# Optimization experiments

Measured on AMD Instinct MI355X. Metric: run time of the kernel, lower is better.

## Reference

```python
import jax, jax.numpy as jnp
import numpy as np

EPS = 1e-5
N, K, C = 32768, 27, 128


def setup_inputs() -> dict:
    key = jax.random.key(0)
    k1, k2, k3, k4 = jax.random.split(key, 4)
    feats = jax.random.normal(k1, (N, C), dtype=jnp.float32)
    # Precomputed kernel-offset neighbor map (MinkowskiEngine kernel map),
    # one input index per (point, kernel offset).
    neighbors = jax.random.randint(k2, (N, K), 0, N, dtype=jnp.int32)
    scale = 1.0 / np.sqrt(K * C)  # fan-in init like sparse conv
    W1 = jax.random.normal(k3, (K, C, C), dtype=jnp.float32) * scale
    W2 = jax.random.normal(k4, (K, C, C), dtype=jnp.float32) * scale
    g1 = jnp.ones((C,), jnp.float32)
    b1 = jnp.zeros((C,), jnp.float32)
    g2 = jnp.ones((C,), jnp.float32)
    b2 = jnp.zeros((C,), jnp.float32)
    return {"feats": feats, "neighbors": neighbors, "W1": W1, "g1": g1,
            "b1": b1, "W2": W2, "g2": g2, "b2": b2}


def _sparse_conv(f, nbr, W):
    # gather-GEMM-scatter: gather neighbor features per kernel offset,
    # contract with that offset's weight, sum over offsets.
    gathered = f[nbr]                      # [N, K, C]
    return jnp.einsum('nkc,kcd->nd', gathered, W)  # [N, C]


def _batch_norm(x, gamma, beta):
    mu = jnp.mean(x, axis=0)
    var = jnp.mean(jnp.square(x - mu), axis=0)
    return (x - mu) * jax.lax.rsqrt(var + EPS) * gamma + beta


def reference(feats, neighbors, W1, g1, b1, W2, g2, b2):
    out = _sparse_conv(feats, neighbors, W1)
    out = jax.nn.relu(_batch_norm(out, g1, b1))
    out = _sparse_conv(out, neighbors, W2)
    out = _batch_norm(out, g2, b2)
    return jax.nn.relu(out + feats)
```

## Files before the change

kernel.cpp:

```cpp
#include <hip/hip_runtime.h>
#include <stdint.h>

#define NPTS 32768
#define KOFF 27
#define CH   128
#define NC   (NPTS*CH)
#define KSPLIT 3
#define KPG  9
#define TILE_M 64
#define NITER (KPG*2)

typedef __attribute__((ext_vector_type(8))) short short8;
typedef __attribute__((ext_vector_type(4))) float f32x4;
typedef unsigned short u16;

__device__ __forceinline__ float bf2f(u16 u) {
    union { uint32_t i; float f; } v; v.i = ((uint32_t)u) << 16; return v.f;
}
__device__ __forceinline__ u16 f2bf(float f) {
    union { float f; uint32_t i; } v; v.f = f;
    return (u16)((v.i + 0x7FFF + ((v.i >> 16) & 1)) >> 16);
}

#define GLDS16(gp, lp) __builtin_amdgcn_global_load_lds( \
    (__attribute__((address_space(1))) void*)(gp),           \
    (__attribute__((address_space(3))) void*)(lp), 16, 0, 0)

__global__ __launch_bounds__(256)
void prep_kernel(const float* __restrict__ W1, const float* __restrict__ W2,
                 u16* __restrict__ W1t, u16* __restrict__ W2t,
                 const float* __restrict__ feats, u16* __restrict__ xbuf,
                 float* __restrict__ stat)
{
    __shared__ u16 t[128*129];
    const int b = blockIdx.x, tid = threadIdx.x;
    if (b < 2*KOFF) {
        if (b == 0) for (int i = tid; i < 512; i += 256) stat[i] = 0.0f;
        const float* src = (b < KOFF) ? W1 + (size_t)b*CH*CH : W2 + (size_t)(b-KOFF)*CH*CH;
        u16* dst         = (b < KOFF) ? W1t + (size_t)b*CH*CH : W2t + (size_t)(b-KOFF)*CH*CH;
        for (int e = tid; e < CH*CH; e += 256) {
            int c = e >> 7, d = e & 127;
            t[d*129 + c] = f2bf(src[e]);
        }
        __syncthreads();
        for (int e = tid; e < CH*CH; e += 256) {
            int d = e >> 7, c = e & 127;
            dst[e] = t[d*129 + c];
        }
    } else {
        size_t e = ((size_t)(b - 2*KOFF) * 256 + tid) * 8;
        float4 a = *(const float4*)(feats + e);
        float4 c = *(const float4*)(feats + e + 4);
        ushort4 lo, hi;
        lo.x = f2bf(a.x); lo.y = f2bf(a.y); lo.z = f2bf(a.z); lo.w = f2bf(a.w);
        hi.x = f2bf(c.x); hi.y = f2bf(c.y); hi.z = f2bf(c.z); hi.w = f2bf(c.w);
        *(ushort4*)(xbuf + e) = lo;
        *(ushort4*)(xbuf + e + 4) = hi;
    }
}

__global__ __launch_bounds__(256, 5)
void ResidualBlock_77498389889548_kernel(const u16* __restrict__ xb,
                                         const int* __restrict__ nbr,
                                         const u16* __restrict__ Wt,
                                         u16* __restrict__ part)
{
    __shared__ __align__(16) u16 A_lds[TILE_M*64];
    __shared__ __align__(16) u16 B_lds[CH*64];
    __shared__ int idx_lds[KPG*TILE_M];

    const int tid = threadIdx.x;
    const int n0  = blockIdx.x * TILE_M;
    const int kg  = blockIdx.y;

    for (int e = tid; e < KPG*TILE_M; e += 256) {
        int kk = e >> 6, r = e & 63;
        int nb = nbr[(size_t)(n0 + r)*KOFF + kg*KPG + kk];
        idx_lds[e] = ((unsigned)nb < (unsigned)NPTS) ? nb : 0;
    }
    __syncthreads();

    const int wave = tid >> 6;
    const int lane = tid & 63;
    const int wrow = (wave >> 1) * 32;
    const int wcol = (wave & 1) * 64;
    const int lm   = lane & 15;
    const int quad = lane >> 4;
    const int l8r  = lane >> 3;
    const int swz  = ((lane & 7) ^ l8r) << 3;

    f32x4 acc[2][4];
    #pragma unroll
    for (int i = 0; i < 2; ++i)
        #pragma unroll
        for (int j = 0; j < 4; ++j)
            #pragma unroll
            for (int r = 0; r < 4; ++r) acc[i][j][r] = 0.0f;

    int aoff[2][2], boff[2][4];
    #pragma unroll
    for (int kc = 0; kc < 2; ++kc) {
        int g = kc*4 + quad;
        #pragma unroll
        for (int i = 0; i < 2; ++i) {
            int row = wrow + i*16 + lm;
            aoff[kc][i] = row*128 + ((g ^ (row & 7)) << 4);
        }
        #pragma unroll
        for (int j = 0; j < 4; ++j) {
            int d = wcol + j*16 + lm;
            boff[kc][j] = d*128 + ((g ^ (d & 7)) << 4);
        }
    }

    const char* Ab = (const char*)A_lds;
    const char* Bb = (const char*)B_lds;

    for (int it = 0; it < NITER; ++it) {
        const int kk = it >> 1;
        const int h  = it & 1;

        #pragma unroll
        for (int j = 0; j < 2; ++j) {
            int row8 = wave*16 + j*8;
            int nb = idx_lds[kk*64 + row8 + l8r];
            GLDS16(xb + (size_t)nb*CH + h*64 + swz, &A_lds[row8*64]);
        }
        const u16* wb = Wt + (size_t)(kg*KPG + kk)*CH*CH + h*64 + swz;
        #pragma unroll
        for (int j = 0; j < 4; ++j) {
            int row8 = wave*32 + j*8;
            GLDS16(wb + (size_t)(row8 + l8r)*CH, &B_lds[row8*64]);
        }
        __syncthreads();

        #pragma unroll
        for (int kc = 0; kc < 2; ++kc) {
            short8 a[2], b[4];
            #pragma unroll
            for (int i = 0; i < 2; ++i) a[i] = *(const short8*)(Ab + aoff[kc][i]);
            #pragma unroll
            for (int j = 0; j < 4; ++j) b[j] = *(const short8*)(Bb + boff[kc][j]);
            #pragma unroll
            for (int i = 0; i < 2; ++i)
                #pragma unroll
                for (int j = 0; j < 4; ++j)
                    acc[i][j] = __builtin_amdgcn_mfma_f32_16x16x32_bf16(a[i], b[j], acc[i][j], 0, 0, 0);
        }
        __syncthreads();
    }

    u16* pb = part + (size_t)kg * NC;
    const int colb = wcol + lm;
    #pragma unroll
    for (int i = 0; i < 2; ++i) {
        #pragma unroll
        for (int r = 0; r < 4; ++r) {
            int row = n0 + wrow + i*16 + quad*4 + r;
            u16* pp = pb + (size_t)row*CH + colb;
            #pragma unroll
            for (int j = 0; j < 4; ++j) pp[j*16] = f2bf(acc[i][j][r]);
        }
    }
}

__global__ __launch_bounds__(256)
void sumstats_kernel(const u16* __restrict__ p0, const u16* __restrict__ p1,
                     const u16* __restrict__ p2, u16* __restrict__ y,
                     float* __restrict__ gsum, float* __restrict__ gsq)
{
    __shared__ float ls[CH], lq[CH];
    const int tid = threadIdx.x;
    const int c8 = (tid & 15) * 8;
    const int r0 = tid >> 4;
    const int b = blockIdx.x;
    if (tid < CH) { ls[tid] = 0.0f; lq[tid] = 0.0f; }
    __syncthreads();

    float s[8], q[8];
    #pragma unroll
    for (int i = 0; i < 8; ++i) { s[i] = 0.0f; q[i] = 0.0f; }

    for (int r = r0; r < 128; r += 16) {
        size_t e = (size_t)(b*128 + r)*CH + c8;
        ushort4 a0 = *(const ushort4*)(p0 + e), a1 = *(const ushort4*)(p0 + e + 4);
        ushort4 b0 = *(const ushort4*)(p1 + e), b1 = *(const ushort4*)(p1 + e + 4);
        ushort4 d0 = *(const ushort4*)(p2 + e), d1 = *(const ushort4*)(p2 + e + 4);
        float v[8];
        v[0] = bf2f(a0.x) + bf2f(b0.x) + bf2f(d0.x);
        v[1] = bf2f(a0.y) + bf2f(b0.y) + bf2f(d0.y);
        v[2] = bf2f(a0.z) + bf2f(b0.z) + bf2f(d0.z);
        v[3] = bf2f(a0.w) + bf2f(b0.w) + bf2f(d0.w);
        v[4] = bf2f(a1.x) + bf2f(b1.x) + bf2f(d1.x);
        v[5] = bf2f(a1.y) + bf2f(b1.y) + bf2f(d1.y);
        v[6] = bf2f(a1.z) + bf2f(b1.z) + bf2f(d1.z);
        v[7] = bf2f(a1.w) + bf2f(b1.w) + bf2f(d1.w);
        ushort4 o0, o1;
        o0.x = f2bf(v[0]); o0.y = f2bf(v[1]); o0.z = f2bf(v[2]); o0.w = f2bf(v[3]);
        o1.x = f2bf(v[4]); o1.y = f2bf(v[5]); o1.z = f2bf(v[6]); o1.w = f2bf(v[7]);
        *(ushort4*)(y + e) = o0;
        *(ushort4*)(y + e + 4) = o1;
        #pragma unroll
        for (int i = 0; i < 8; ++i) { s[i] += v[i]; q[i] += v[i]*v[i]; }
    }
    #pragma unroll
    for (int i = 0; i < 8; ++i) {
        atomicAdd(&ls[c8 + i], s[i]);
        atomicAdd(&lq[c8 + i], q[i]);
    }
    __syncthreads();
    if (tid < CH) {
        atomicAdd(&gsum[tid], ls[tid]);
        atomicAdd(&gsq[tid],  lq[tid]);
    }
}

__global__ __launch_bounds__(256)
void norm_relu_kernel(const u16* __restrict__ y, const float* __restrict__ sums,
                      const float* __restrict__ sumsq, const float* __restrict__ gam,
                      const float* __restrict__ bet, u16* __restrict__ xo)
{
    __shared__ float sc[128], sh[128];
    const int tid = threadIdx.x;
    if (tid < 128) {
        float mu  = sums[tid] * (1.0f/NPTS);
        float var = fmaxf(sumsq[tid] * (1.0f/NPTS) - mu*mu, 0.0f);
        float rs  = rsqrtf(var + 1e-5f);
        float s   = rs * gam[tid];
        sc[tid] = s; sh[tid] = bet[tid] - mu*s;
    }
    __syncthreads();
    size_t e = ((size_t)blockIdx.x*256 + tid) * 8;
    int c0 = (int)(e & 127);
    ushort4 lo = *(const ushort4*)(y + e);
    ushort4 hi = *(const ushort4*)(y + e + 4);
    ushort4 o0, o1;
    o0.x = f2bf(fmaxf(bf2f(lo.x)*sc[c0+0] + sh[c0+0], 0.0f));
    o0.y = f2bf(fmaxf(bf2f(lo.y)*sc[c0+1] + sh[c0+1], 0.0f));
    o0.z = f2bf(fmaxf(bf2f(lo.z)*sc[c0+2] + sh[c0+2], 0.0f));
    o0.w = f2bf(fmaxf(bf2f(lo.w)*sc[c0+3] + sh[c0+3], 0.0f));
    o1.x = f2bf(fmaxf(bf2f(hi.x)*sc[c0+4] + sh[c0+4], 0.0f));
    o1.y = f2bf(fmaxf(bf2f(hi.y)*sc[c0+5] + sh[c0+5], 0.0f));
    o1.z = f2bf(fmaxf(bf2f(hi.z)*sc[c0+6] + sh[c0+6], 0.0f));
    o1.w = f2bf(fmaxf(bf2f(hi.w)*sc[c0+7] + sh[c0+7], 0.0f));
    *(ushort4*)(xo + e) = o0;
    *(ushort4*)(xo + e + 4) = o1;
}

__global__ __launch_bounds__(256)
void final_kernel(const u16* __restrict__ y, const float* __restrict__ sums,
                  const float* __restrict__ sumsq, const float* __restrict__ gam,
                  const float* __restrict__ bet, const float* __restrict__ feats,
                  float* __restrict__ out)
{
    __shared__ float sc[128], sh[128];
    const int tid = threadIdx.x;
    if (tid < 128) {
        float mu  = sums[tid] * (1.0f/NPTS);
        float var = fmaxf(sumsq[tid] * (1.0f/NPTS) - mu*mu, 0.0f);
        float rs  = rsqrtf(var + 1e-5f);
        float s   = rs * gam[tid];
        sc[tid] = s; sh[tid] = bet[tid] - mu*s;
    }
    __syncthreads();
    size_t e = ((size_t)blockIdx.x*256 + tid) * 4;
    int c0 = (int)(e & 127);
    ushort4 in = *(const ushort4*)(y + e);
    float4 ft = *(const float4*)(feats + e);
    float4 o;
    o.x = fmaxf(bf2f(in.x)*sc[c0+0] + sh[c0+0] + ft.x, 0.0f);
    o.y = fmaxf(bf2f(in.y)*sc[c0+1] + sh[c0+1] + ft.y, 0.0f);
    o.z = fmaxf(bf2f(in.z)*sc[c0+2] + sh[c0+2] + ft.z, 0.0f);
    o.w = fmaxf(bf2f(in.w)*sc[c0+3] + sh[c0+3] + ft.w, 0.0f);
    *(float4*)(out + e) = o;
}

extern "C" void kernel_launch(void* const* d_in, const int* in_sizes, int n_in,
                              void* d_out, int out_size, void* d_ws, size_t ws_size,
                              hipStream_t stream)
{
    const float* feats = (const float*)d_in[0];
    const int*   nbr   = (const int*)d_in[1];
    const float* W1    = (const float*)d_in[2];
    const float* g1    = (const float*)d_in[3];
    const float* b1    = (const float*)d_in[4];
    const float* W2    = (const float*)d_in[5];
    const float* g2    = (const float*)d_in[6];
    const float* b2    = (const float*)d_in[7];
    float* out = (float*)d_out;

    char* ws = (char*)d_ws;
    u16*   xbuf = (u16*)ws;
    u16*   prt  = xbuf + (size_t)NC;
    u16*   ybuf = prt + (size_t)3*NC;
    u16*   W1t  = ybuf + (size_t)NC;
    u16*   W2t  = W1t + (size_t)KOFF*CH*CH;
    float* stat = (float*)(W2t + (size_t)KOFF*CH*CH);

    prep_kernel<<<dim3(2*KOFF + NC/2048), 256, 0, stream>>>(W1, W2, W1t, W2t, feats, xbuf, stat);

    ResidualBlock_77498389889548_kernel<<<dim3(NPTS/TILE_M, KSPLIT), 256, 0, stream>>>(
        xbuf, nbr, W1t, prt);
    sumstats_kernel<<<dim3(NPTS/128), 256, 0, stream>>>(
        prt, prt + (size_t)NC, prt + (size_t)2*NC, ybuf, stat, stat + 128);
    norm_relu_kernel<<<dim3(NC/2048), 256, 0, stream>>>(ybuf, stat, stat + 128, g1, b1, xbuf);

    ResidualBlock_77498389889548_kernel<<<dim3(NPTS/TILE_M, KSPLIT), 256, 0, stream>>>(
        xbuf, nbr, W2t, prt);
    sumstats_kernel<<<dim3(NPTS/128), 256, 0, stream>>>(
        prt, prt + (size_t)NC, prt + (size_t)2*NC, ybuf, stat + 256, stat + 384);
    final_kernel<<<dim3(NC/1024), 256, 0, stream>>>(ybuf, stat + 256, stat + 384, g2, b2, feats, out);
}
```

Baseline: 222.5 us.

## Fuse partial-sum, BN statistics and normalize via grid barrier; shrink index LDS

Merges the sumstats and normalize/final kernels into one persistent 256-block kernel. Each block keeps its summed tile in LDS, joins a global atomic-counter barrier once the batch statistics are complete, then normalizes straight from LDS. This drops the ybuf round trip through global memory and one launch per BN. It also stores neighbor indices as u16 and raises the GEMM's waves-per-EU hint from 5 to 6 for occupancy. The grid barrier relies on all 256 blocks being co-resident, and the counters are zeroed in the prep kernel each call.

```diff
diff --git a/kernel.cpp b/kernel.cpp
--- a/kernel.cpp
+++ b/kernel.cpp
@@ -9,6 +9,7 @@
 #define KPG  9
 #define TILE_M 64
 #define NITER (KPG*2)
+#define RBLK  256
 
 typedef __attribute__((ext_vector_type(8))) short short8;
 typedef __attribute__((ext_vector_type(4))) float f32x4;
@@ -35,7 +36,7 @@
     __shared__ u16 t[128*129];
     const int b = blockIdx.x, tid = threadIdx.x;
     if (b < 2*KOFF) {
-        if (b == 0) for (int i = tid; i < 512; i += 256) stat[i] = 0.0f;
+        if (b == 0) for (int i = tid; i < 640; i += 256) stat[i] = 0.0f;
         const float* src = (b < KOFF) ? W1 + (size_t)b*CH*CH : W2 + (size_t)(b-KOFF)*CH*CH;
         u16* dst         = (b < KOFF) ? W1t + (size_t)b*CH*CH : W2t + (size_t)(b-KOFF)*CH*CH;
         for (int e = tid; e < CH*CH; e += 256) {
@@ -59,7 +60,7 @@
     }
 }
 
-__global__ __launch_bounds__(256, 5)
+__global__ __launch_bounds__(256, 6)
 void ResidualBlock_77498389889548_kernel(const u16* __restrict__ xb,
                                          const int* __restrict__ nbr,
                                          const u16* __restrict__ Wt,
@@ -67,7 +68,7 @@
 {
     __shared__ __align__(16) u16 A_lds[TILE_M*64];
     __shared__ __align__(16) u16 B_lds[CH*64];
-    __shared__ int idx_lds[KPG*TILE_M];
+    __shared__ u16 idx_lds[KPG*TILE_M];
 
     const int tid = threadIdx.x;
     const int n0  = blockIdx.x * TILE_M;
@@ -76,7 +77,7 @@
     for (int e = tid; e < KPG*TILE_M; e += 256) {
         int kk = e >> 6, r = e & 63;
         int nb = nbr[(size_t)(n0 + r)*KOFF + kg*KPG + kk];
-        idx_lds[e] = ((unsigned)nb < (unsigned)NPTS) ? nb : 0;
+        idx_lds[e] = (u16)(((unsigned)nb < (unsigned)NPTS) ? nb : 0);
     }
     __syncthreads();
 
@@ -123,7 +124,7 @@
         #pragma unroll
         for (int j = 0; j < 2; ++j) {
             int row8 = wave*16 + j*8;
-            int nb = idx_lds[kk*64 + row8 + l8r];
+            int nb = (int)idx_lds[kk*64 + row8 + l8r];
             GLDS16(xb + (size_t)nb*CH + h*64 + swz, &A_lds[row8*64]);
         }
         const u16* wb = Wt + (size_t)(kg*KPG + kk)*CH*CH + h*64 + swz;
@@ -164,115 +165,112 @@
     }
 }
 
+#define FUSED_PROLOGUE(p0, p1, p2, gsum, gsq, ctr)                              \
+    __shared__ u16 vbuf[128*CH];                                     \
+    __shared__ float ls[CH], lq[CH];                                            \
+    const int tid = threadIdx.x;                                                \
+    const int b = blockIdx.x;                                                   \
+    const int c8 = (tid & 15) * 8;                                              \
+    const int r0 = tid >> 4;                                                    \
+    if (tid < CH) { ls[tid] = 0.0f; lq[tid] = 0.0f; }                           \
+    __syncthreads();                                                            \
+    {                                                                           \
+        float s[8], q[8];                                                       \
+        _Pragma("unroll") for (int i = 0; i < 8; ++i) { s[i]=0.0f; q[i]=0.0f; } \
+        for (int i = 0; i < 8; ++i) {                                           \
+            int r = r0 + i*16;                                                  \
+            size_t e = (size_t)(b*128 + r)*CH + c8;                             \
+            ushort4 a0 = *(const ushort4*)(p0 + e), a1 = *(const ushort4*)(p0 + e + 4); \
+            ushort4 b0 = *(const ushort4*)(p1 + e), b1 = *(const ushort4*)(p1 + e + 4); \
+            ushort4 d0 = *(const ushort4*)(p2 + e), d1 = *(const ushort4*)(p2 + e + 4); \
+            float v[8];                                                         \
+            v[0]=bf2f(a0.x)+bf2f(b0.x)+bf2f(d0.x); v[1]=bf2f(a0.y)+bf2f(b0.y)+bf2f(d0.y); \
+            v[2]=bf2f(a0.z)+bf2f(b0.z)+bf2f(d0.z); v[3]=bf2f(a0.w)+bf2f(b0.w)+bf2f(d0.w); \
+            v[4]=bf2f(a1.x)+bf2f(b1.x)+bf2f(d1.x); v[5]=bf2f(a1.y)+bf2f(b1.y)+bf2f(d1.y); \
+            v[6]=bf2f(a1.z)+bf2f(b1.z)+bf2f(d1.z); v[7]=bf2f(a1.w)+bf2f(b1.w)+bf2f(d1.w); \
+            u16* vp = &vbuf[r*CH + c8];                                         \
+            _Pragma("unroll") for (int j = 0; j < 8; ++j) vp[j] = f2bf(v[j]);   \
+            _Pragma("unroll") for (int j = 0; j < 8; ++j) { s[j]+=v[j]; q[j]+=v[j]*v[j]; } \
+        }                                                                       \
+        _Pragma("unroll") for (int j = 0; j < 8; ++j) {                         \
+            atomicAdd(&ls[c8 + j], s[j]); atomicAdd(&lq[c8 + j], q[j]);         \
+        }                                                                       \
+    }                                                                           \
+    __syncthreads();                                                            \
+    if (tid < CH) { atomicAdd(&gsum[tid], ls[tid]); atomicAdd(&gsq[tid], lq[tid]); } \
+    __syncthreads();                                                            \
+    if (tid == 0) {                                                             \
+        __threadfence();                                                        \
+        __hip_atomic_fetch_add(ctr, 1u, __ATOMIC_RELEASE, __HIP_MEMORY_SCOPE_AGENT); \
+        while (__hip_atomic_load(ctr, __ATOMIC_ACQUIRE, __HIP_MEMORY_SCOPE_AGENT) < (unsigned)RBLK) \
+            __builtin_amdgcn_s_sleep(8);                                        \
+    }                                                                           \
+    __syncthreads();                                                            \
+    if (tid < CH) {                                                             \
+        float su = __hip_atomic_load(&gsum[tid], __ATOMIC_RELAXED, __HIP_MEMORY_SCOPE_AGENT); \
+        float sq = __hip_atomic_load(&gsq[tid],  __ATOMIC_RELAXED, __HIP_MEMORY_SCOPE_AGENT); \
+        float mu  = su * (1.0f/NPTS);                                           \
+        float var = fmaxf(sq * (1.0f/NPTS) - mu*mu, 0.0f);                      \
+        float rs  = rsqrtf(var + 1e-5f);                                        \
+        float sf  = rs * gam[tid];                                              \
+        ls[tid] = sf; lq[tid] = bet[tid] - mu*sf;                   \
+    }                                                                           \
+    __syncthreads();
+
 __global__ __launch_bounds__(256)
-void sumstats_kernel(const u16* __restrict__ p0, const u16* __restrict__ p1,
-                     const u16* __restrict__ p2, u16* __restrict__ y,
-                     float* __restrict__ gsum, float* __restrict__ gsq)
-{
-    __shared__ float ls[CH], lq[CH];
-    const int tid = threadIdx.x;
-    const int c8 = (tid & 15) * 8;
-    const int r0 = tid >> 4;
-    const int b = blockIdx.x;
-    if (tid < CH) { ls[tid] = 0.0f; lq[tid] = 0.0f; }
-    __syncthreads();
-
-    float s[8], q[8];
-    #pragma unroll
-    for (int i = 0; i < 8; ++i) { s[i] = 0.0f; q[i] = 0.0f; }
-
-    for (int r = r0; r < 128; r += 16) {
+void fused_norm_kernel(const u16* __restrict__ p0, const u16* __restrict__ p1,
+                       const u16* __restrict__ p2,
+                       float* __restrict__ gsum, float* __restrict__ gsq,
+                       unsigned* __restrict__ ctr,
+                       const float* __restrict__ gam, const float* __restrict__ bet,
+                       u16* __restrict__ xo)
+{
+    FUSED_PROLOGUE(p0, p1, p2, gsum, gsq, ctr)
+    for (int i = 0; i < 8; ++i) {
+        int r = r0 + i*16;
         size_t e = (size_t)(b*128 + r)*CH + c8;
-        ushort4 a0 = *(const ushort4*)(p0 + e), a1 = *(const ushort4*)(p0 + e + 4);
-        ushort4 b0 = *(const ushort4*)(p1 + e), b1 = *(const ushort4*)(p1 + e + 4);
-        ushort4 d0 = *(const ushort4*)(p2 + e), d1 = *(const ushort4*)(p2 + e + 4);
-        float v[8];
-        v[0] = bf2f(a0.x) + bf2f(b0.x) + bf2f(d0.x);
-        v[1] = bf2f(a0.y) + bf2f(b0.y) + bf2f(d0.y);
-        v[2] = bf2f(a0.z) + bf2f(b0.z) + bf2f(d0.z);
-        v[3] = bf2f(a0.w) + bf2f(b0.w) + bf2f(d0.w);
-        v[4] = bf2f(a1.x) + bf2f(b1.x) + bf2f(d1.x);
-        v[5] = bf2f(a1.y) + bf2f(b1.y) + bf2f(d1.y);
-        v[6] = bf2f(a1.z) + bf2f(b1.z) + bf2f(d1.z);
-        v[7] = bf2f(a1.w) + bf2f(b1.w) + bf2f(d1.w);
+        const u16* vp = &vbuf[r*CH + c8];
         ushort4 o0, o1;
-        o0.x = f2bf(v[0]); o0.y = f2bf(v[1]); o0.z = f2bf(v[2]); o0.w = f2bf(v[3]);
-        o1.x = f2bf(v[4]); o1.y = f2bf(v[5]); o1.z = f2bf(v[6]); o1.w = f2bf(v[7]);
-        *(ushort4*)(y + e) = o0;
-        *(ushort4*)(y + e + 4) = o1;
-        #pragma unroll
-        for (int i = 0; i < 8; ++i) { s[i] += v[i]; q[i] += v[i]*v[i]; }
-    }
-    #pragma unroll
+        o0.x = f2bf(fmaxf(bf2f(vp[0])*ls[c8+0] + lq[c8+0], 0.0f));
+        o0.y = f2bf(fmaxf(bf2f(vp[1])*ls[c8+1] + lq[c8+1], 0.0f));
+        o0.z = f2bf(fmaxf(bf2f(vp[2])*ls[c8+2] + lq[c8+2], 0.0f));
+        o0.w = f2bf(fmaxf(bf2f(vp[3])*ls[c8+3] + lq[c8+3], 0.0f));
+        o1.x = f2bf(fmaxf(bf2f(vp[4])*ls[c8+4] + lq[c8+4], 0.0f));
+        o1.y = f2bf(fmaxf(bf2f(vp[5])*ls[c8+5] + lq[c8+5], 0.0f));
+        o1.z = f2bf(fmaxf(bf2f(vp[6])*ls[c8+6] + lq[c8+6], 0.0f));
+        o1.w = f2bf(fmaxf(bf2f(vp[7])*ls[c8+7] + lq[c8+7], 0.0f));
+        *(ushort4*)(xo + e) = o0;
+        *(ushort4*)(xo + e + 4) = o1;
+    }
+}
+
+__global__ __launch_bounds__(256)
+void fused_final_kernel(const u16* __restrict__ p0, const u16* __restrict__ p1,
+                        const u16* __restrict__ p2,
+                        float* __restrict__ gsum, float* __restrict__ gsq,
+                        unsigned* __restrict__ ctr,
+                        const float* __restrict__ gam, const float* __restrict__ bet,
+                        const float* __restrict__ feats, float* __restrict__ out)
+{
+    FUSED_PROLOGUE(p0, p1, p2, gsum, gsq, ctr)
     for (int i = 0; i < 8; ++i) {
-        atomicAdd(&ls[c8 + i], s[i]);
-        atomicAdd(&lq[c8 + i], q[i]);
-    }
-    __syncthreads();
-    if (tid < CH) {
-        atomicAdd(&gsum[tid], ls[tid]);
-        atomicAdd(&gsq[tid],  lq[tid]);
-    }
-}
-
-__global__ __launch_bounds__(256)
-void norm_relu_kernel(const u16* __restrict__ y, const float* __restrict__ sums,
-                      const float* __restrict__ sumsq, const float* __restrict__ gam,
-                      const float* __restrict__ bet, u16* __restrict__ xo)
-{
-    __shared__ float sc[128], sh[128];
-    const int tid = threadIdx.x;
-    if (tid < 128) {
-        float mu  = sums[tid] * (1.0f/NPTS);
-        float var = fmaxf(sumsq[tid] * (1.0f/NPTS) - mu*mu, 0.0f);
-        float rs  = rsqrtf(var + 1e-5f);
-        float s   = rs * gam[tid];
-        sc[tid] = s; sh[tid] = bet[tid] - mu*s;
-    }
-    __syncthreads();
-    size_t e = ((size_t)blockIdx.x*256 + tid) * 8;
-    int c0 = (int)(e & 127);
-    ushort4 lo = *(const ushort4*)(y + e);
-    ushort4 hi = *(const ushort4*)(y + e + 4);
-    ushort4 o0, o1;
-    o0.x = f2bf(fmaxf(bf2f(lo.x)*sc[c0+0] + sh[c0+0], 0.0f));
-    o0.y = f2bf(fmaxf(bf2f(lo.y)*sc[c0+1] + sh[c0+1], 0.0f));
-    o0.z = f2bf(fmaxf(bf2f(lo.z)*sc[c0+2] + sh[c0+2], 0.0f));
-    o0.w = f2bf(fmaxf(bf2f(lo.w)*sc[c0+3] + sh[c0+3], 0.0f));
-    o1.x = f2bf(fmaxf(bf2f(hi.x)*sc[c0+4] + sh[c0+4], 0.0f));
-    o1.y = f2bf(fmaxf(bf2f(hi.y)*sc[c0+5] + sh[c0+5], 0.0f));
-    o1.z = f2bf(fmaxf(bf2f(hi.z)*sc[c0+6] + sh[c0+6], 0.0f));
-    o1.w = f2bf(fmaxf(bf2f(hi.w)*sc[c0+7] + sh[c0+7], 0.0f));
-    *(ushort4*)(xo + e) = o0;
-    *(ushort4*)(xo + e + 4) = o1;
-}
-
-__global__ __launch_bounds__(256)
-void final_kernel(const u16* __restrict__ y, const float* __restrict__ sums,
-                  const float* __restrict__ sumsq, const float* __restrict__ gam,
-                  const float* __restrict__ bet, const float* __restrict__ feats,
-                  float* __restrict__ out)
-{
-    __shared__ float sc[128], sh[128];
-    const int tid = threadIdx.x;
-    if (tid < 128) {
-        float mu  = sums[tid] * (1.0f/NPTS);
-        float var = fmaxf(sumsq[tid] * (1.0f/NPTS) - mu*mu, 0.0f);
-        float rs  = rsqrtf(var + 1e-5f);
-        float s   = rs * gam[tid];
-        sc[tid] = s; sh[tid] = bet[tid] - mu*s;
-    }
-    __syncthreads();
-    size_t e = ((size_t)blockIdx.x*256 + tid) * 4;
-    int c0 = (int)(e & 127);
-    ushort4 in = *(const ushort4*)(y + e);
-    float4 ft = *(const float4*)(feats + e);
-    float4 o;
-    o.x = fmaxf(bf2f(in.x)*sc[c0+0] + sh[c0+0] + ft.x, 0.0f);
-    o.y = fmaxf(bf2f(in.y)*sc[c0+1] + sh[c0+1] + ft.y, 0.0f);
-    o.z = fmaxf(bf2f(in.z)*sc[c0+2] + sh[c0+2] + ft.z, 0.0f);
-    o.w = fmaxf(bf2f(in.w)*sc[c0+3] + sh[c0+3] + ft.w, 0.0f);
-    *(float4*)(out + e) = o;
+        int r = r0 + i*16;
+        size_t e = (size_t)(b*128 + r)*CH + c8;
+        const u16* vp = &vbuf[r*CH + c8];
+        float4 f0 = *(const float4*)(feats + e);
+        float4 f1 = *(const float4*)(feats + e + 4);
+        float4 o0, o1;
+        o0.x = fmaxf(bf2f(vp[0])*ls[c8+0] + lq[c8+0] + f0.x, 0.0f);
+        o0.y = fmaxf(bf2f(vp[1])*ls[c8+1] + lq[c8+1] + f0.y, 0.0f);
+        o0.z = fmaxf(bf2f(vp[2])*ls[c8+2] + lq[c8+2] + f0.z, 0.0f);
+        o0.w = fmaxf(bf2f(vp[3])*ls[c8+3] + lq[c8+3] + f0.w, 0.0f);
+        o1.x = fmaxf(bf2f(vp[4])*ls[c8+4] + lq[c8+4] + f1.x, 0.0f);
+        o1.y = fmaxf(bf2f(vp[5])*ls[c8+5] + lq[c8+5] + f1.y, 0.0f);
+        o1.z = fmaxf(bf2f(vp[6])*ls[c8+6] + lq[c8+6] + f1.z, 0.0f);
+        o1.w = fmaxf(bf2f(vp[7])*ls[c8+7] + lq[c8+7] + f1.w, 0.0f);
+        *(float4*)(out + e) = o0;
+        *(float4*)(out + e + 4) = o1;
+    }
 }
 
 extern "C" void kernel_launch(void* const* d_in, const int* in_sizes, int n_in,
@@ -292,22 +290,20 @@
     char* ws = (char*)d_ws;
     u16*   xbuf = (u16*)ws;
     u16*   prt  = xbuf + (size_t)NC;
-    u16*   ybuf = prt + (size_t)3*NC;
-    u16*   W1t  = ybuf + (size_t)NC;
+    u16*   W1t  = prt + (size_t)3*NC;
     u16*   W2t  = W1t + (size_t)KOFF*CH*CH;
     float* stat = (float*)(W2t + (size_t)KOFF*CH*CH);
+    unsigned* ctrs = (unsigned*)(stat + 512);
 
     prep_kernel<<<dim3(2*KOFF + NC/2048), 256, 0, stream>>>(W1, W2, W1t, W2t, feats, xbuf, stat);
 
     ResidualBlock_77498389889548_kernel<<<dim3(NPTS/TILE_M, KSPLIT), 256, 0, stream>>>(
         xbuf, nbr, W1t, prt);
-    sumstats_kernel<<<dim3(NPTS/128), 256, 0, stream>>>(
-        prt, prt + (size_t)NC, prt + (size_t)2*NC, ybuf, stat, stat + 128);
-    norm_relu_kernel<<<dim3(NC/2048), 256, 0, stream>>>(ybuf, stat, stat + 128, g1, b1, xbuf);
+    fused_norm_kernel<<<dim3(RBLK), 256, 0, stream>>>(
+        prt, prt + (size_t)NC, prt + (size_t)2*NC, stat, stat + 128, ctrs, g1, b1, xbuf);
 
     ResidualBlock_77498389889548_kernel<<<dim3(NPTS/TILE_M, KSPLIT), 256, 0, stream>>>(
         xbuf, nbr, W2t, prt);
-    sumstats_kernel<<<dim3(NPTS/128), 256, 0, stream>>>(
-        prt, prt + (size_t)NC, prt + (size_t)2*NC, ybuf, stat + 256, stat + 384);
-    final_kernel<<<dim3(NC/1024), 256, 0, stream>>>(ybuf, stat + 256, stat + 384, g2, b2, feats, out);
-}
+    fused_final_kernel<<<dim3(RBLK), 256, 0, stream>>>(
+        prt, prt + (size_t)NC, prt + (size_t)2*NC, stat + 256, stat + 384, ctrs + 1, g2, b2, feats, out);
+}
```

Result: slower. 308.8 us (+38.8%).
